# Performance work log

Hardware: AMD Instinct MI355X
Metric: run time of the kernel (lower is better)

Reference implementation:

```python
import jax, jax.numpy as jnp
import numpy as np

S = 30.0
ML = 0.4
MS = 0.1
N, D, C = 8192, 1024, 10240

def setup_inputs() -> dict:
    key = jax.random.key(0)
    k1, k2, k3 = jax.random.split(key, 3)
    x = jax.random.normal(k1, (N, D), dtype=jnp.float32)
    labels = jax.random.randint(k2, (N,), 0, C, dtype=jnp.int64)
    # xavier_uniform for weight (C, D)
    limit = float(np.sqrt(6.0 / (C + D)))
    weight = jax.random.uniform(k3, (C, D), dtype=jnp.float32, minval=-limit, maxval=limit)
    return {"x": x, "labels": labels, "weight": weight}

def _l2norm(v, axis):
    # matches F.normalize (eps=1e-12)
    n = jnp.sqrt(jnp.sum(v * v, axis=axis, keepdims=True))
    return v / jnp.maximum(n, 1e-12)

def reference(x, labels, weight):
    # cosine logits, clamped to [-1, 1]
    wf = jnp.clip(_l2norm(x, 1) @ _l2norm(weight, 1).T, -1.0, 1.0)  # (N, C)
    # per-sample additive margin: ml if label<=5 (real) else ms (fake)
    m = jnp.where(labels <= 5, ML, MS).astype(wf.dtype)  # (N,)
    target = jnp.take_along_axis(wf, labels[:, None], axis=1)[:, 0]  # wf[i, labels[i]]
    numerator = S * (target - m)
    # sum over j != label of exp(s*wf[i,j]) == full sum minus the label term
    exp_all = jnp.exp(S * wf)
    excl_sum = jnp.sum(exp_all, axis=1) - jnp.exp(S * target)
    denominator = jnp.exp(numerator) + excl_sum
    L = numerator - jnp.log(denominator)
    return -jnp.mean(L)
```

## Files before the change

### kernel.cpp

```cpp
#include <hip/hip_runtime.h>
#include <hip/hip_bf16.h>

#define N_ROWS 8192
#define DIM    1024
#define NCLS   10240
#define S_SCALE 30.0f
#define M_LARGE 0.4f
#define M_SMALL 0.1f

typedef __attribute__((ext_vector_type(4))) int   i32x4;

#define GLD16(gp, lp) __builtin_amdgcn_global_load_lds( \
    (const __attribute__((address_space(1))) unsigned int*)(gp), \
    (__attribute__((address_space(3))) unsigned int*)(lp), 16, 0, 0)

__global__ void prep_kernel(const float* __restrict__ x, const float* __restrict__ w,
                            float* __restrict__ fx, float* __restrict__ fw,
                            float* __restrict__ gsum,
                            signed char* __restrict__ xq, signed char* __restrict__ wq){
    int b = blockIdx.x;
    bool isx = (b < N_ROWS);
    int r = isx ? b : b - N_ROWS;
    const float4* src = (const float4*)((isx ? x : w) + (size_t)r * DIM);
    float4 v = src[threadIdx.x];
    float ss = v.x*v.x + v.y*v.y + v.z*v.z + v.w*v.w;
    float am = fmaxf(fmaxf(fabsf(v.x), fabsf(v.y)), fmaxf(fabsf(v.z), fabsf(v.w)));
    #pragma unroll
    for (int o = 32; o; o >>= 1){
        ss += __shfl_down(ss, o);
        am  = fmaxf(am, __shfl_down(am, o));
    }
    __shared__ float pss[4], pam[4];
    int lane = threadIdx.x & 63, wid = threadIdx.x >> 6;
    if (lane == 0){ pss[wid] = ss; pam[wid] = am; }
    __syncthreads();
    float t    = pss[0] + pss[1] + pss[2] + pss[3];
    float amax = fmaxf(fmaxf(pam[0], pam[1]), fmaxf(pam[2], pam[3]));
    float inv  = 1.0f / fmaxf(sqrtf(t), 1e-12f);
    float s    = fmaxf(amax, 1e-20f) * (1.0f/127.0f);
    float rs   = 127.0f / fmaxf(amax, 1e-20f);
    int q0 = __float2int_rn(v.x * rs), q1 = __float2int_rn(v.y * rs);
    int q2 = __float2int_rn(v.z * rs), q3 = __float2int_rn(v.w * rs);
    unsigned int pk = (q0 & 0xff) | ((q1 & 0xff) << 8) | ((q2 & 0xff) << 16) | ((q3 & 0xff) << 24);
    ((unsigned int*)((isx ? xq : wq) + (size_t)r * DIM))[threadIdx.x] = pk;
    if (threadIdx.x == 0){
        if (isx){ fx[r] = s * inv; gsum[r] = 0.0f; }
        else      fw[r] = s * inv;
    }
}

#define BM 256
#define BN 256
#define BKB 128
#define NT (DIM/BKB)
#define GRID_X (NCLS/BN)
#define GRID_Y (N_ROWS/BM)
#define NWG (GRID_X*GRID_Y)

__global__ __launch_bounds__(1024) void gemm_kernel(
        const signed char* __restrict__ xq, const signed char* __restrict__ wq,
        const float* __restrict__ fx, const float* __restrict__ fw,
        const int* __restrict__ labels,
        float* __restrict__ gsum, float* __restrict__ tgt){
    __shared__ __align__(16) unsigned char As[2][BM*BKB];
    __shared__ __align__(16) unsigned char Bs[2][BN*BKB];
    __shared__ float sumrow[BM];
    __shared__ int   lab_s[BM];

    int tid = threadIdx.x;
    int bid = blockIdx.x;
    int swz = (bid & 7) * (NWG/8) + (bid >> 3);
    int by = swz / GRID_X, bx = swz % GRID_X;
    int row0 = by * BM, col0 = bx * BN;
    int wid = tid >> 6, lane = tid & 63;
    int wm = wid >> 2, wn = wid & 3;
    int g = lane >> 4, l16 = lane & 15;

    if (tid < BM){ sumrow[tid] = 0.f; lab_s[tid] = labels[row0 + tid]; }

    int srow = tid >> 3;
    int csrc = (tid & 7) ^ (srow & 7);
    const signed char* gA = xq + (size_t)(row0 + srow) * DIM + csrc * 16;
    const signed char* gB = wq + (size_t)(col0 + srow) * DIM + csrc * 16;
    int ldso = srow * BKB + (tid & 7) * 16;

    i32x4 acc[4][4] = {};

    GLD16(gA,                     &As[0][ldso]);
    GLD16(gA + (size_t)128*DIM,   &As[0][128*BKB + ldso]);
    GLD16(gB,                     &Bs[0][ldso]);
    GLD16(gB + (size_t)128*DIM,   &Bs[0][128*BKB + ldso]);
    __syncthreads();

    for (int kt = 0; kt < NT; ++kt){
        int b = kt & 1, nb = b ^ 1;
        if (kt + 1 < NT){
            int kn = (kt + 1) * BKB;
            GLD16(gA + kn,                     &As[nb][ldso]);
            GLD16(gA + kn + (size_t)128*DIM,   &As[nb][128*BKB + ldso]);
            GLD16(gB + kn,                     &Bs[nb][ldso]);
            GLD16(gB + kn + (size_t)128*DIM,   &Bs[nb][128*BKB + ldso]);
        }

        #pragma unroll
        for (int kk = 0; kk < 2; ++kk){
            i32x4 af[4], bfv[4];
            #pragma unroll
            for (int m = 0; m < 4; ++m){
                int r = wm*64 + m*16 + l16;
                af[m] = *(const i32x4*)&As[b][r*BKB + (((kk*4+g) ^ (r & 7)) << 4)];
            }
            #pragma unroll
            for (int n = 0; n < 4; ++n){
                int r = wn*64 + n*16 + l16;
                bfv[n] = *(const i32x4*)&Bs[b][r*BKB + (((kk*4+g) ^ (r & 7)) << 4)];
            }
            #pragma unroll
            for (int m = 0; m < 4; ++m)
                #pragma unroll
                for (int n = 0; n < 4; ++n)
                    acc[m][n] = __builtin_amdgcn_mfma_i32_16x16x64_i8(af[m], bfv[n], acc[m][n], 0, 0, 0);
        }

        asm volatile("s_waitcnt vmcnt(0)" ::: "memory");
        __syncthreads();
    }

    float fwv[4];
    #pragma unroll
    for (int n = 0; n < 4; ++n) fwv[n] = fw[col0 + wn*64 + n*16 + l16];
    #pragma unroll
    for (int m = 0; m < 4; ++m){
        #pragma unroll
        for (int rg = 0; rg < 4; ++rg){
            int rl = wm*64 + m*16 + g*4 + rg;
            float fxr = fx[row0 + rl];
            int lab = lab_s[rl];
            float v = 0.f;
            #pragma unroll
            for (int n = 0; n < 4; ++n){
                float c = (float)acc[m][n][rg] * fxr * fwv[n];
                c = fminf(fmaxf(c, -1.f), 1.f);
                v += __expf(S_SCALE * c);
                if (lab == col0 + wn*64 + n*16 + l16) tgt[row0 + rl] = c;
            }
            v += __shfl_xor(v, 1);
            v += __shfl_xor(v, 2);
            v += __shfl_xor(v, 4);
            v += __shfl_xor(v, 8);
            if (l16 == 0) atomicAdd(&sumrow[rl], v);
        }
    }
    __syncthreads();
    if (tid < BM) atomicAdd(&gsum[row0 + tid], sumrow[tid]);
}

__global__ void finalize_kernel(const float* __restrict__ tgt, const float* __restrict__ gsum,
                                const int* __restrict__ labels, float* __restrict__ out){
    double local = 0.0;
    for (int i = threadIdx.x; i < N_ROWS; i += 1024){
        float tv = tgt[i];
        float m  = (labels[i] <= 5) ? M_LARGE : M_SMALL;
        float numer = S_SCALE * (tv - m);
        float excl  = gsum[i] - __expf(S_SCALE * tv);
        float denom = __expf(numer) + excl;
        float L = numer - logf(denom);
        local += (double)L;
    }
    #pragma unroll
    for (int o = 32; o; o >>= 1) local += __shfl_down(local, o);
    __shared__ double part[16];
    int lane = threadIdx.x & 63, wid = threadIdx.x >> 6;
    if (lane == 0) part[wid] = local;
    __syncthreads();
    if (threadIdx.x == 0){
        double s = 0.0;
        #pragma unroll
        for (int p = 0; p < 16; ++p) s += part[p];
        out[0] = (float)(-s / (double)N_ROWS);
    }
}

extern "C" void kernel_launch(void* const* d_in, const int* in_sizes, int n_in,
                              void* d_out, int out_size, void* d_ws, size_t ws_size,
                              hipStream_t stream) {
    const float* x      = (const float*)d_in[0];
    const int*   labels = (const int*)  d_in[1];
    const float* w      = (const float*)d_in[2];

    float* ws    = (float*)d_ws;
    float* fx    = ws;
    float* fw    = fx    + N_ROWS;
    float* tgt   = fw    + NCLS;
    float* gsum  = tgt   + N_ROWS;
    signed char* xq = (signed char*)(gsum + N_ROWS);
    signed char* wq = xq + (size_t)N_ROWS * DIM;

    prep_kernel<<<N_ROWS + NCLS, 256, 0, stream>>>(x, w, fx, fw, gsum, xq, wq);
    gemm_kernel<<<NWG, 1024, 0, stream>>>(xq, wq, fx, fw, labels, gsum, tgt);
    finalize_kernel<<<1, 1024, 0, stream>>>(tgt, gsum, labels, (float*)d_out);
}
```

Before: 133.8 us.

## Make int8 GEMM persistent and prefetch next tile during epilogue

The grid of 1280 tile workgroups becomes 256 persistent workgroups that each process 5 tiles. The first K-slice of the next tile is prefetched into shared memory during the last K-step of the current one, so global loads overlap the MFMA tail and the exp/reduction epilogue. This is meant to cut launch and tail costs and the pipeline-fill bubble at each tile start. In exchange it adds extra barriers per tile, and with 256 workgroups on 256 CUs any imbalance in the tile order is exposed directly.

```diff
diff --git a/kernel.cpp b/kernel.cpp
--- a/kernel.cpp
+++ b/kernel.cpp
@@ -56,6 +56,8 @@
 #define GRID_X (NCLS/BN)
 #define GRID_Y (N_ROWS/BM)
 #define NWG (GRID_X*GRID_Y)
+#define NBLK 256
+#define TPB (NWG/NBLK)
 
 __global__ __launch_bounds__(1024) void gemm_kernel(
         const signed char* __restrict__ xq, const signed char* __restrict__ wq,
@@ -69,90 +71,118 @@
 
     int tid = threadIdx.x;
     int bid = blockIdx.x;
-    int swz = (bid & 7) * (NWG/8) + (bid >> 3);
-    int by = swz / GRID_X, bx = swz % GRID_X;
-    int row0 = by * BM, col0 = bx * BN;
     int wid = tid >> 6, lane = tid & 63;
     int wm = wid >> 2, wn = wid & 3;
     int g = lane >> 4, l16 = lane & 15;
 
-    if (tid < BM){ sumrow[tid] = 0.f; lab_s[tid] = labels[row0 + tid]; }
-
     int srow = tid >> 3;
     int csrc = (tid & 7) ^ (srow & 7);
+    int ldso = srow * BKB + (tid & 7) * 16;
+
+    #define TILEBASE(T, R, C) { int swz_ = (bid & 7)*(NWG/8) + (bid >> 3) + 32*(T); \
+                                R = (swz_ / GRID_X) * BM; C = (swz_ % GRID_X) * BN; }
+
+    int row0, col0;
+    TILEBASE(0, row0, col0);
     const signed char* gA = xq + (size_t)(row0 + srow) * DIM + csrc * 16;
     const signed char* gB = wq + (size_t)(col0 + srow) * DIM + csrc * 16;
-    int ldso = srow * BKB + (tid & 7) * 16;
-
-    i32x4 acc[4][4] = {};
-
-    GLD16(gA,                     &As[0][ldso]);
-    GLD16(gA + (size_t)128*DIM,   &As[0][128*BKB + ldso]);
-    GLD16(gB,                     &Bs[0][ldso]);
-    GLD16(gB + (size_t)128*DIM,   &Bs[0][128*BKB + ldso]);
+
+    GLD16(gA,                   &As[0][ldso]);
+    GLD16(gA + (size_t)128*DIM, &As[0][128*BKB + ldso]);
+    GLD16(gB,                   &Bs[0][ldso]);
+    GLD16(gB + (size_t)128*DIM, &Bs[0][128*BKB + ldso]);
+    if (tid < BM){ sumrow[tid] = 0.f; lab_s[tid] = labels[row0 + tid]; }
     __syncthreads();
 
-    for (int kt = 0; kt < NT; ++kt){
-        int b = kt & 1, nb = b ^ 1;
-        if (kt + 1 < NT){
-            int kn = (kt + 1) * BKB;
-            GLD16(gA + kn,                     &As[nb][ldso]);
-            GLD16(gA + kn + (size_t)128*DIM,   &As[nb][128*BKB + ldso]);
-            GLD16(gB + kn,                     &Bs[nb][ldso]);
-            GLD16(gB + kn + (size_t)128*DIM,   &Bs[nb][128*BKB + ldso]);
-        }
-
+    for (int t = 0; t < TPB; ++t){
+        int nrow0 = 0, ncol0 = 0;
+        const signed char* ngA = gA;
+        const signed char* ngB = gB;
+        if (t + 1 < TPB){
+            TILEBASE(t + 1, nrow0, ncol0);
+            ngA = xq + (size_t)(nrow0 + srow) * DIM + csrc * 16;
+            ngB = wq + (size_t)(ncol0 + srow) * DIM + csrc * 16;
+        }
+
+        i32x4 acc[4][4] = {};
+
+        for (int kt = 0; kt < NT; ++kt){
+            int b = kt & 1, nb = b ^ 1;
+            if (kt + 1 < NT){
+                int kn = (kt + 1) * BKB;
+                GLD16(gA + kn,                   &As[nb][ldso]);
+                GLD16(gA + kn + (size_t)128*DIM, &As[nb][128*BKB + ldso]);
+                GLD16(gB + kn,                   &Bs[nb][ldso]);
+                GLD16(gB + kn + (size_t)128*DIM, &Bs[nb][128*BKB + ldso]);
+            } else if (t + 1 < TPB){
+                GLD16(ngA,                   &As[nb][ldso]);
+                GLD16(ngA + (size_t)128*DIM, &As[nb][128*BKB + ldso]);
+                GLD16(ngB,                   &Bs[nb][ldso]);
+                GLD16(ngB + (size_t)128*DIM, &Bs[nb][128*BKB + ldso]);
+            }
+
+            #pragma unroll
+            for (int kk = 0; kk < 2; ++kk){
+                i32x4 af[4], bfv[4];
+                #pragma unroll
+                for (int m = 0; m < 4; ++m){
+                    int r = wm*64 + m*16 + l16;
+                    af[m] = *(const i32x4*)&As[b][r*BKB + (((kk*4+g) ^ (r & 7)) << 4)];
+                }
+                #pragma unroll
+                for (int n = 0; n < 4; ++n){
+                    int r = wn*64 + n*16 + l16;
+                    bfv[n] = *(const i32x4*)&Bs[b][r*BKB + (((kk*4+g) ^ (r & 7)) << 4)];
+                }
+                #pragma unroll
+                for (int m = 0; m < 4; ++m)
+                    #pragma unroll
+                    for (int n = 0; n < 4; ++n)
+                        acc[m][n] = __builtin_amdgcn_mfma_i32_16x16x64_i8(af[m], bfv[n], acc[m][n], 0, 0, 0);
+            }
+
+            if (kt + 1 < NT){
+                asm volatile("s_waitcnt vmcnt(0)" ::: "memory");
+                __syncthreads();
+            }
+        }
+
+        float fwv[4];
         #pragma unroll
-        for (int kk = 0; kk < 2; ++kk){
-            i32x4 af[4], bfv[4];
+        for (int n = 0; n < 4; ++n) fwv[n] = fw[col0 + wn*64 + n*16 + l16];
+        #pragma unroll
+        for (int m = 0; m < 4; ++m){
             #pragma unroll
-            for (int m = 0; m < 4; ++m){
-                int r = wm*64 + m*16 + l16;
-                af[m] = *(const i32x4*)&As[b][r*BKB + (((kk*4+g) ^ (r & 7)) << 4)];
-            }
-            #pragma unroll
-            for (int n = 0; n < 4; ++n){
-                int r = wn*64 + n*16 + l16;
-                bfv[n] = *(const i32x4*)&Bs[b][r*BKB + (((kk*4+g) ^ (r & 7)) << 4)];
-            }
-            #pragma unroll
-            for (int m = 0; m < 4; ++m)
-                #pragma unroll
-                for (int n = 0; n < 4; ++n)
-                    acc[m][n] = __builtin_amdgcn_mfma_i32_16x16x64_i8(af[m], bfv[n], acc[m][n], 0, 0, 0);
-        }
-
-        asm volatile("s_waitcnt vmcnt(0)" ::: "memory");
+            for (int rg = 0; rg < 4; ++rg){
+                int rl = wm*64 + m*16 + g*4 + rg;
+                float fxr = fx[row0 + rl];
+                int lab = lab_s[rl];
+                float v = 0.f;
+                #pragma unroll
+                for (int n = 0; n < 4; ++n){
+                    float c = (float)acc[m][n][rg] * fxr * fwv[n];
+                    c = fminf(fmaxf(c, -1.f), 1.f);
+                    v += __expf(S_SCALE * c);
+                    if (lab == col0 + wn*64 + n*16 + l16) tgt[row0 + rl] = c;
+                }
+                v += __shfl_xor(v, 1);
+                v += __shfl_xor(v, 2);
+                v += __shfl_xor(v, 4);
+                v += __shfl_xor(v, 8);
+                if (l16 == 0) atomicAdd(&sumrow[rl], v);
+            }
+        }
         __syncthreads();
-    }
-
-    float fwv[4];
-    #pragma unroll
-    for (int n = 0; n < 4; ++n) fwv[n] = fw[col0 + wn*64 + n*16 + l16];
-    #pragma unroll
-    for (int m = 0; m < 4; ++m){
-        #pragma unroll
-        for (int rg = 0; rg < 4; ++rg){
-            int rl = wm*64 + m*16 + g*4 + rg;
-            float fxr = fx[row0 + rl];
-            int lab = lab_s[rl];
-            float v = 0.f;
-            #pragma unroll
-            for (int n = 0; n < 4; ++n){
-                float c = (float)acc[m][n][rg] * fxr * fwv[n];
-                c = fminf(fmaxf(c, -1.f), 1.f);
-                v += __expf(S_SCALE * c);
-                if (lab == col0 + wn*64 + n*16 + l16) tgt[row0 + rl] = c;
-            }
-            v += __shfl_xor(v, 1);
-            v += __shfl_xor(v, 2);
-            v += __shfl_xor(v, 4);
-            v += __shfl_xor(v, 8);
-            if (l16 == 0) atomicAdd(&sumrow[rl], v);
-        }
-    }
-    __syncthreads();
-    if (tid < BM) atomicAdd(&gsum[row0 + tid], sumrow[tid]);
+        if (tid < BM) atomicAdd(&gsum[row0 + tid], sumrow[tid]);
+
+        if (t + 1 < TPB){
+            row0 = nrow0; col0 = ncol0; gA = ngA; gB = ngB;
+            asm volatile("s_waitcnt vmcnt(0)" ::: "memory");
+            __syncthreads();
+            if (tid < BM){ sumrow[tid] = 0.f; lab_s[tid] = labels[row0 + tid]; }
+            __syncthreads();
+        }
+    }
 }
 
 __global__ void finalize_kernel(const float* __restrict__ tgt, const float* __restrict__ gsum,
@@ -197,6 +227,6 @@
     signed char* wq = xq + (size_t)N_ROWS * DIM;
 
     prep_kernel<<<N_ROWS + NCLS, 256, 0, stream>>>(x, w, fx, fw, gsum, xq, wq);
-    gemm_kernel<<<NWG, 1024, 0, stream>>>(xq, wq, fx, fw, labels, gsum, tgt);
+    gemm_kernel<<<NBLK, 1024, 0, stream>>>(xq, wq, fx, fw, labels, gsum, tgt);
     finalize_kernel<<<1, 1024, 0, stream>>>(tgt, gsum, labels, (float*)d_out);
 }
```

Result: slower. 139.4 us (+4.1%).
